# Kernel tuning notes

Hardware: AMD Instinct MI355X
Metric: run time of the kernel (lower is better)

Reference implementation:

```python
import jax, jax.numpy as jnp
import numpy as np

B, C, L = 32, 512, 16          # batch, clauses per CNF, max literals per clause
D, H, P = 256, 1024, 16        # clause_hidden_dim, hidden_size, prefix_tokens
NH, NL = 8, 4                  # adapter_heads, adapter_layers
MAXV = 512                     # max_variables


def _ln(x, w, b, eps=1e-5):
    m = jnp.mean(x, axis=-1, keepdims=True)
    v = jnp.mean(jnp.square(x - m), axis=-1, keepdims=True)
    return (x - m) * jax.lax.rsqrt(v + eps) * w + b


def _mha(q, k, v, w_in, b_in, w_out, b_out, nh):
    E = q.shape[-1]
    dh = E // nh
    wq, wk, wv = jnp.split(w_in, 3, axis=0)
    bq, bk, bv = jnp.split(b_in, 3, axis=0)

    def heads(x, w, b):
        y = x @ w.T + b
        return y.reshape(x.shape[0], x.shape[1], nh, dh).transpose(0, 2, 1, 3)

    qh, kh, vh = heads(q, wq, bq), heads(k, wk, bk), heads(v, wv, bv)
    att = jax.nn.softmax(jnp.einsum('bhqd,bhkd->bhqk', qh, kh) * (1.0 / np.sqrt(dh)), axis=-1)
    o = jnp.einsum('bhqk,bhkd->bhqd', att, vh).transpose(0, 2, 1, 3).reshape(q.shape[0], q.shape[1], E)
    return o @ w_out.T + b_out


def setup_inputs() -> dict:
    key = jax.random.key(0)
    ks = jax.random.split(key, 16)
    s = 0.02
    var_idx = jax.random.randint(ks[0], (B, C, L), 0, MAXV + 1)
    sign_idx = jax.random.randint(ks[1], (B, C, L), 1, 3)   # 1=positive literal, 2=negative
    lens = jax.random.randint(ks[2], (B, C), 1, L + 1)      # ragged clause lengths >= 1
    lit_mask = jnp.arange(L)[None, None, :] < lens[..., None]
    inp = dict(var_idx=var_idx, sign_idx=sign_idx, lit_mask=lit_mask)
    inp['var_emb'] = jax.random.normal(ks[3], (MAXV + 1, D)) * s
    inp['sign_emb'] = jax.random.normal(ks[4], (3, D)) * s
    inp['litpos_emb'] = jax.random.normal(ks[5], (L, D)) * s
    inp['clausepos_emb'] = jax.random.normal(ks[6], (C, D)) * s
    inp['enc_in_w'] = jax.random.normal(ks[7], (NL, 3 * D, D)) * s
    inp['enc_in_b'] = jnp.zeros((NL, 3 * D))
    inp['enc_out_w'] = jax.random.normal(ks[8], (NL, D, D)) * s
    inp['enc_out_b'] = jnp.zeros((NL, D))
    inp['enc_ff1_w'] = jax.random.normal(ks[9], (NL, 4 * D, D)) * s
    inp['enc_ff1_b'] = jnp.zeros((NL, 4 * D))
    inp['enc_ff2_w'] = jax.random.normal(ks[10], (NL, D, 4 * D)) * s
    inp['enc_ff2_b'] = jnp.zeros((NL, D))
    inp['enc_n1_w'] = jnp.ones((NL, D))
    inp['enc_n1_b'] = jnp.zeros((NL, D))
    inp['enc_n2_w'] = jnp.ones((NL, D))
    inp['enc_n2_b'] = jnp.zeros((NL, D))
    inp['th_ln_w'] = jnp.ones((D,))
    inp['th_ln_b'] = jnp.zeros((D,))
    inp['th_w'] = jax.random.normal(ks[11], (H, D)) * s
    inp['th_b'] = jnp.zeros((H,))
    inp['pq'] = jax.random.normal(ks[12], (P, H))
    inp['pa_in_w'] = jax.random.normal(ks[13], (3 * H, H)) * s
    inp['pa_in_b'] = jnp.zeros((3 * H,))
    inp['pa_out_w'] = jax.random.normal(ks[14], (H, H)) * s
    inp['pa_out_b'] = jnp.zeros((H,))
    inp['pn_w'] = jnp.ones((H,))
    inp['pn_b'] = jnp.zeros((H,))
    return inp


def reference(var_idx, sign_idx, lit_mask, var_emb, sign_emb, litpos_emb, clausepos_emb,
              enc_in_w, enc_in_b, enc_out_w, enc_out_b, enc_ff1_w, enc_ff1_b,
              enc_ff2_w, enc_ff2_b, enc_n1_w, enc_n1_b, enc_n2_w, enc_n2_b,
              th_ln_w, th_ln_b, th_w, th_b, pq, pa_in_w, pa_in_b, pa_out_w, pa_out_b,
              pn_w, pn_b):
    # literal states [B,C,L,D]: four embedding gathers fused into one expression
    lit = (var_emb[var_idx] + sign_emb[sign_idx]
           + litpos_emb[None, None, :, :] + clausepos_emb[None, :, None, :])
    m = lit_mask[..., None].astype(lit.dtype)
    x = jnp.sum(lit * m, axis=2) / jnp.sum(m, axis=2)   # masked mean-pool -> [B,C,D]
    for i in range(NL):  # PyTorch post-norm TransformerEncoderLayer, gelu (exact)
        a = _mha(x, x, x, enc_in_w[i], enc_in_b[i], enc_out_w[i], enc_out_b[i], NH)
        x = _ln(x + a, enc_n1_w[i], enc_n1_b[i])
        f = jax.nn.gelu(x @ enc_ff1_w[i].T + enc_ff1_b[i], approximate=False) @ enc_ff2_w[i].T + enc_ff2_b[i]
        x = _ln(x + f, enc_n2_w[i], enc_n2_b[i])
    ch = _ln(x, th_ln_w, th_ln_b) @ th_w.T + th_b       # to_hidden -> [B,C,H]
    q = jnp.broadcast_to(pq[None], (ch.shape[0], P, H))
    pref = _mha(q, ch, ch, pa_in_w, pa_in_b, pa_out_w, pa_out_b, NH)
    return _ln(pref + q, pn_w, pn_b)                    # [B,P,H]
```

## Files before the change

### kernel.cpp

```cpp
#include <hip/hip_runtime.h>
#include <hip/hip_bf16.h>

typedef unsigned short u16;
typedef unsigned int u32;
typedef __attribute__((ext_vector_type(8))) short short8;
typedef __attribute__((ext_vector_type(4))) float floatx4;

#define BB 32
#define CC 512
#define LL 16
#define DD 256
#define HH 1024
#define PP 16
#define NLAY 4

__device__ __forceinline__ float bf2f(u16 u) {
  u32 x = ((u32)u) << 16; float f; __builtin_memcpy(&f, &x, 4); return f;
}
__device__ __forceinline__ u16 f2bf(float f) {
  __hip_bfloat16 h = __float2bfloat16(f);
  u16 r; __builtin_memcpy(&r, &h, 2); return r;
}
__device__ __forceinline__ void gload_lds16(const u16* g, u16* l) {
  __builtin_amdgcn_global_load_lds(
      (const __attribute__((address_space(1))) void*)g,
      (__attribute__((address_space(3))) void*)l, 16, 0, 0);
}

__global__ __launch_bounds__(256) void cvt_kernel(
    const float* __restrict__ s0, const float* __restrict__ s1,
    const float* __restrict__ s2, const float* __restrict__ s3,
    const float* __restrict__ s4, const float* __restrict__ s5,
    const float* __restrict__ s6, const float* __restrict__ s7,
    const float* __restrict__ s8, const float* __restrict__ s9,
    const float* __restrict__ s10, const float* __restrict__ s11,
    u16* __restrict__ dst)
{
  const float* srcs[12] = {s0, s1, s2, s3, s4, s5, s6, s7, s8, s9, s10, s11};
  const int pfx[12] = {786432, 1048576, 2097152, 3145728, 3407872, 6553600, 7602176,
                       7618560, 7749888, 7750656, 7754752, 7885824};
  int e = (blockIdx.x * 256 + threadIdx.x) * 4;
  int seg = 0;
  while (e >= pfx[seg]) seg++;
  int start = seg ? pfx[seg - 1] : 0;
  float4 f = *(const float4*)(srcs[seg] + (e - start));
  u16 o[4] = {f2bf(f.x), f2bf(f.y), f2bf(f.z), f2bf(f.w)};
  *(uint2*)(dst + e) = *(const uint2*)o;
}

__global__ __launch_bounds__(256) void thwT_kernel(
    const float* __restrict__ thw, u16* __restrict__ out)
{
  __shared__ float tile[32][33];
  int bx = blockIdx.x & 7, by = blockIdx.x >> 3;
  int tx = threadIdx.x & 31, ty = threadIdx.x >> 5;
  #pragma unroll
  for (int i = 0; i < 4; ++i) {
    int h = by * 32 + ty + i * 8, d = bx * 32 + tx;
    tile[ty + i * 8][tx] = thw[h * 256 + d];
  }
  __syncthreads();
  #pragma unroll
  for (int i = 0; i < 4; ++i) {
    int d = bx * 32 + ty + i * 8, h = by * 32 + tx;
    out[d * 1024 + h] = f2bf(tile[tx][ty + i * 8]);
  }
}

__global__ __launch_bounds__(256) void bT_kernel(
    const u16* __restrict__ in, u16* __restrict__ out)
{
  __shared__ u16 tile[32][33];
  int bx = blockIdx.x & 7, by = blockIdx.x >> 3;
  int tx = threadIdx.x & 31, ty = threadIdx.x >> 5;
  #pragma unroll
  for (int i = 0; i < 4; ++i) {
    int hd = by * 32 + ty + i * 8, c = bx * 32 + tx;
    tile[ty + i * 8][tx] = in[hd * 256 + c];
  }
  __syncthreads();
  #pragma unroll
  for (int i = 0; i < 4; ++i) {
    int c = bx * 32 + ty + i * 8, hd = by * 32 + tx;
    out[c * 1024 + hd] = tile[tx][ty + i * 8];
  }
}

__global__ __launch_bounds__(256) void qc_kernel(
    const u16* __restrict__ qh, const u16* __restrict__ wckT, u16* __restrict__ qcg)
{
  int h = blockIdx.x;
  int t = threadIdx.x, lane = t & 63, w = t >> 6;
  int mrow = lane & 15, quad = lane >> 4;
  const floatx4 zf = (floatx4){0.f, 0.f, 0.f, 0.f};
  floatx4 acc[4] = {zf, zf, zf, zf};
  #pragma unroll
  for (int kk = 0; kk < 4; ++kk) {
    short8 af = *(const short8*)(qh + (size_t)mrow * 1024 + h * 128 + kk * 32 + quad * 8);
    #pragma unroll
    for (int ct = 0; ct < 4; ++ct) {
      int c = w * 64 + ct * 16 + mrow;
      short8 bf = *(const short8*)(wckT + (size_t)c * 1024 + h * 128 + kk * 32 + quad * 8);
      acc[ct] = __builtin_amdgcn_mfma_f32_16x16x32_bf16(af, bf, acc[ct], 0, 0, 0);
    }
  }
  #pragma unroll
  for (int ct = 0; ct < 4; ++ct)
    #pragma unroll
    for (int r = 0; r < 4; ++r)
      qcg[((size_t)h * 16 + quad * 4 + r) * 256 + w * 64 + ct * 16 + mrow] = f2bf(acc[ct][r]);
}

__global__ __launch_bounds__(256) void biasfold_kernel(
    const u16* __restrict__ Wkv, const float* __restrict__ thb,
    const float* __restrict__ paib, float* __restrict__ out)
{
  int wv = threadIdx.x >> 6, lane = threadIdx.x & 63;
  int n = blockIdx.x * 4 + wv;
  const u16* wr = Wkv + (size_t)n * 1024;
  float s = 0.f;
  #pragma unroll
  for (int i = 0; i < 16; ++i) {
    int h = i * 64 + lane;
    s += bf2f(wr[h]) * thb[h];
  }
  #pragma unroll
  for (int off = 32; off; off >>= 1) s += __shfl_xor(s, off);
  if (!lane) out[n] = s + paib[1024 + n];
}

__global__ __launch_bounds__(256) void redk_kernel(
    const float* __restrict__ part, const float* __restrict__ bias,
    const float* __restrict__ res, float* __restrict__ outf, u16* __restrict__ outb,
    int N, int nz, int total, int flags)
{
  int idx = (blockIdx.x * 256 + threadIdx.x) * 4;
  if (idx >= total) return;
  float4 a = *(const float4*)(part + idx);
  for (int z = 1; z < nz; ++z) {
    float4 b = *(const float4*)(part + (size_t)z * total + idx);
    a.x += b.x; a.y += b.y; a.z += b.z; a.w += b.w;
  }
  int row = idx / N, col = idx - row * N;
  float v4[4] = {a.x, a.y, a.z, a.w};
  #pragma unroll
  for (int i = 0; i < 4; ++i) {
    if (bias) v4[i] += bias[col + i];
    if (res) v4[i] += res[(size_t)((flags & 4) ? (row & 15) : row) * N + col + i];
  }
  if (outf) {
    *(float4*)(outf + idx) = *(const float4*)v4;
  } else {
    u16 o[4] = {f2bf(v4[0]), f2bf(v4[1]), f2bf(v4[2]), f2bf(v4[3])};
    *(uint2*)(outb + idx) = *(const uint2*)o;
  }
}

__global__ __launch_bounds__(256) void embed_kernel(
    const int* __restrict__ vi, const int* __restrict__ si, const int* __restrict__ mk,
    const u16* __restrict__ veb, const u16* __restrict__ seb,
    const u16* __restrict__ lpeb, const u16* __restrict__ cpeb,
    u16* __restrict__ xb)
{
  int t = threadIdx.x;
  int bc = blockIdx.x * 2 + (t >> 7);
  int c = bc & (CC - 1);
  int dl = (t & 127) * 2;
  int base = bc * LL;
  float a0 = 0.f, a1 = 0.f; int cnt = 0;
  #pragma unroll
  for (int l = 0; l < LL; ++l) {
    if (mk[base + l]) {
      int v = vi[base + l], s = si[base + l];
      u32 vv = *(const u32*)&veb[v * DD + dl];
      u32 sv = *(const u32*)&seb[s * DD + dl];
      u32 lv = *(const u32*)&lpeb[l * DD + dl];
      a0 += bf2f((u16)vv) + bf2f((u16)sv) + bf2f((u16)lv);
      a1 += bf2f((u16)(vv >> 16)) + bf2f((u16)(sv >> 16)) + bf2f((u16)(lv >> 16));
      cnt++;
    }
  }
  u32 cv = *(const u32*)&cpeb[c * DD + dl];
  float inv = 1.f / (float)cnt;
  u32 pk = (u32)f2bf(a0 * inv + bf2f((u16)cv)) | ((u32)f2bf(a1 * inv + bf2f((u16)(cv >> 16))) << 16);
  *(u32*)&xb[(size_t)bc * DD + dl] = pk;
}

template<int NC, bool GELU, bool LN, bool DLN>
__global__ __launch_bounds__(256) void gwide_kernel(
    const u16* __restrict__ A, const u16* __restrict__ W, const float* __restrict__ bias,
    const u16* __restrict__ resb, const float* __restrict__ gam, const float* __restrict__ bet,
    const float* __restrict__ gam2, const float* __restrict__ bet2,
    u16* __restrict__ out, int N, int K)
{
  constexpr int NT = NC / 32;
  constexpr int NT4 = NC / 64;
  __shared__ __align__(16) u16 As[32 * 64];
  __shared__ __align__(16) u16 Ws[NC * 64];
  __shared__ float sred[32][4][2];
  __shared__ float sred2[32][4][2];
  int t = threadIdx.x, lane = t & 63, w = t >> 6;
  int mrow = lane & 15, quad = lane >> 4;
  int bn0 = blockIdx.x * NC, bm0 = blockIdx.y * 32;

  int rA = t >> 3, gcA = (t & 7) ^ (rA & 7);
  const u16* gAp = A + (size_t)(bm0 + rA) * K + gcA * 8;
  u16* lAp = As + (w * 64) * 8;
  const u16* gW0 = W + (size_t)(bn0 + rA) * K + gcA * 8;
  u16* lW0 = Ws + (w * 64) * 8;

  floatx4 acc[2][NT4];
  #pragma unroll
  for (int mi = 0; mi < 2; ++mi)
    #pragma unroll
    for (int nt = 0; nt < NT4; ++nt) acc[mi][nt] = (floatx4){0.f, 0.f, 0.f, 0.f};

  for (int k0 = 0; k0 < K; k0 += 64) {
    __syncthreads();
    gload_lds16(gAp, lAp); gAp += 64;
    #pragma unroll
    for (int i = 0; i < NT; ++i)
      gload_lds16(gW0 + (size_t)i * 32 * K, lW0 + i * 2048);
    gW0 += 64;
    __syncthreads();
    #pragma unroll
    for (int ks = 0; ks < 2; ++ks) {
      int sw = ((ks * 4 + quad) ^ (mrow & 7)) * 8;
      short8 af0 = *(const short8*)&As[mrow * 64 + sw];
      short8 af1 = *(const short8*)&As[(16 + mrow) * 64 + sw];
      #pragma unroll
      for (int nt = 0; nt < NT4; ++nt) {
        int rw = w * (NC / 4) + nt * 16 + mrow;
        short8 bf = *(const short8*)&Ws[rw * 64 + sw];
        acc[0][nt] = __builtin_amdgcn_mfma_f32_16x16x32_bf16(af0, bf, acc[0][nt], 0, 0, 0);
        acc[1][nt] = __builtin_amdgcn_mfma_f32_16x16x32_bf16(af1, bf, acc[1][nt], 0, 0, 0);
      }
    }
  }

  if constexpr (LN) {
    float val[2][NT4][4];
    float bv[NT4];
    #pragma unroll
    for (int nt = 0; nt < NT4; ++nt) bv[nt] = bias[w * 64 + nt * 16 + mrow];
    #pragma unroll
    for (int mi = 0; mi < 2; ++mi) {
      #pragma unroll
      for (int r = 0; r < 4; ++r) {
        int gm = bm0 + mi * 16 + quad * 4 + r;
        float sr = 0.f, s2r = 0.f;
        #pragma unroll
        for (int nt = 0; nt < NT4; ++nt) {
          int gn = w * 64 + nt * 16 + mrow;
          float v = acc[mi][nt][r] + bv[nt] + bf2f(resb[(size_t)gm * 256 + gn]);
          val[mi][nt][r] = v; sr += v; s2r += v * v;
        }
        sr += __shfl_xor(sr, 1); s2r += __shfl_xor(s2r, 1);
        sr += __shfl_xor(sr, 2); s2r += __shfl_xor(s2r, 2);
        sr += __shfl_xor(sr, 4); s2r += __shfl_xor(s2r, 4);
        sr += __shfl_xor(sr, 8); s2r += __shfl_xor(s2r, 8);
        if (mrow == 0) { sred[mi * 16 + quad * 4 + r][w][0] = sr; sred[mi * 16 + quad * 4 + r][w][1] = s2r; }
      }
    }
    __syncthreads();
    #pragma unroll
    for (int mi = 0; mi < 2; ++mi) {
      #pragma unroll
      for (int r = 0; r < 4; ++r) {
        int lrow = mi * 16 + quad * 4 + r;
        float S  = sred[lrow][0][0] + sred[lrow][1][0] + sred[lrow][2][0] + sred[lrow][3][0];
        float S2 = sred[lrow][0][1] + sred[lrow][1][1] + sred[lrow][2][1] + sred[lrow][3][1];
        float mean = S * (1.f / 256.f);
        float var = S2 * (1.f / 256.f) - mean * mean;
        float inv = rsqrtf(var + 1e-5f);
        float sr2 = 0.f, s2r2 = 0.f;
        #pragma unroll
        for (int nt = 0; nt < NT4; ++nt) {
          int gn = w * 64 + nt * 16 + mrow;
          float y = (val[mi][nt][r] - mean) * inv * gam[gn] + bet[gn];
          val[mi][nt][r] = y;
          if constexpr (DLN) { sr2 += y; s2r2 += y * y; }
          else out[(size_t)(bm0 + lrow) * 256 + gn] = f2bf(y);
        }
        if constexpr (DLN) {
          sr2 += __shfl_xor(sr2, 1); s2r2 += __shfl_xor(s2r2, 1);
          sr2 += __shfl_xor(sr2, 2); s2r2 += __shfl_xor(s2r2, 2);
          sr2 += __shfl_xor(sr2, 4); s2r2 += __shfl_xor(s2r2, 4);
          sr2 += __shfl_xor(sr2, 8); s2r2 += __shfl_xor(s2r2, 8);
          if (mrow == 0) { sred2[lrow][w][0] = sr2; sred2[lrow][w][1] = s2r2; }
        }
      }
    }
    if constexpr (DLN) {
      __syncthreads();
      #pragma unroll
      for (int mi = 0; mi < 2; ++mi) {
        #pragma unroll
        for (int r = 0; r < 4; ++r) {
          int lrow = mi * 16 + quad * 4 + r;
          float S  = sred2[lrow][0][0] + sred2[lrow][1][0] + sred2[lrow][2][0] + sred2[lrow][3][0];
          float S2 = sred2[lrow][0][1] + sred2[lrow][1][1] + sred2[lrow][2][1] + sred2[lrow][3][1];
          float mean = S * (1.f / 256.f);
          float var = S2 * (1.f / 256.f) - mean * mean;
          float inv = rsqrtf(var + 1e-5f);
          #pragma unroll
          for (int nt = 0; nt < NT4; ++nt) {
            int gn = w * 64 + nt * 16 + mrow;
            float z = (val[mi][nt][r] - mean) * inv * gam2[gn] + bet2[gn];
            out[(size_t)(bm0 + lrow) * 256 + gn] = f2bf(z);
          }
        }
      }
    }
  } else {
    #pragma unroll
    for (int nt = 0; nt < NT4; ++nt) {
      int gn = bn0 + w * (NC / 4) + nt * 16 + mrow;
      float bv = bias[gn];
      #pragma unroll
      for (int mi = 0; mi < 2; ++mi) {
        #pragma unroll
        for (int r = 0; r < 4; ++r) {
          int gm = bm0 + mi * 16 + quad * 4 + r;
          float v = acc[mi][nt][r] + bv;
          if (GELU) v = 0.5f * v * (1.f + erff(v * 0.70710678118654752f));
          out[(size_t)gm * N + gn] = f2bf(v);
        }
      }
    }
  }
}

template<bool DLN>
__global__ __launch_bounds__(512) void ffu_kernel(
    const u16* __restrict__ A, const u16* __restrict__ W1, const float* __restrict__ b1,
    const u16* __restrict__ W2, const float* __restrict__ b2,
    const u16* __restrict__ resb,
    const float* __restrict__ gam, const float* __restrict__ bet,
    const float* __restrict__ gam2, const float* __restrict__ bet2,
    u16* __restrict__ out)
{
  __shared__ __align__(16) u16 As[4096];
  __shared__ __align__(16) u16 Ws[16384];
  __shared__ __align__(16) u16 Hs[4 * 4096];
  int t = threadIdx.x, lane = t & 63, w = t >> 6;
  int mrow = lane & 15, quad = lane >> 4;
  int rh = w >> 2, wc = w & 3;
  int bm0 = blockIdx.x * 64;
  int rA = t >> 3, gcA = (t & 7) ^ (rA & 7);

  floatx4 yacc[2][4];
  #pragma unroll
  for (int mi = 0; mi < 2; ++mi)
    #pragma unroll
    for (int nt = 0; nt < 4; ++nt) yacc[mi][nt] = (floatx4){0.f, 0.f, 0.f, 0.f};

  for (int nq = 0; nq < 4; ++nq) {
    floatx4 hacc[2][4];
    #pragma unroll
    for (int mi = 0; mi < 2; ++mi)
      #pragma unroll
      for (int nt = 0; nt < 4; ++nt) hacc[mi][nt] = (floatx4){0.f, 0.f, 0.f, 0.f};
    for (int kt = 0; kt < 4; ++kt) {
      __syncthreads();
      gload_lds16(A + (size_t)(bm0 + rA) * 256 + kt * 64 + gcA * 8, As + (w * 64) * 8);
      #pragma unroll
      for (int i = 0; i < 4; ++i)
        gload_lds16(W1 + (size_t)(nq * 256 + i * 64 + rA) * 256 + kt * 64 + gcA * 8,
                    Ws + i * 4096 + (w * 64) * 8);
      __syncthreads();
      #pragma unroll
      for (int ks = 0; ks < 2; ++ks) {
        int sw = ((ks * 4 + quad) ^ (mrow & 7)) * 8;
        short8 af0 = *(const short8*)&As[(rh * 32 + mrow) * 64 + sw];
        short8 af1 = *(const short8*)&As[(rh * 32 + 16 + mrow) * 64 + sw];
        #pragma unroll
        for (int nt = 0; nt < 4; ++nt) {
          short8 bf = *(const short8*)&Ws[(wc * 64 + nt * 16 + mrow) * 64 + sw];
          hacc[0][nt] = __builtin_amdgcn_mfma_f32_16x16x32_bf16(af0, bf, hacc[0][nt], 0, 0, 0);
          hacc[1][nt] = __builtin_amdgcn_mfma_f32_16x16x32_bf16(af1, bf, hacc[1][nt], 0, 0, 0);
        }
      }
    }
    {
      float bv1[4];
      #pragma unroll
      for (int nt = 0; nt < 4; ++nt) bv1[nt] = b1[nq * 256 + wc * 64 + nt * 16 + mrow];
      #pragma unroll
      for (int mi = 0; mi < 2; ++mi) {
        #pragma unroll
        for (int nt = 0; nt < 4; ++nt) {
          int g = nt * 2 + (mrow >> 3);
          #pragma unroll
          for (int r = 0; r < 4; ++r) {
            int row = rh * 32 + mi * 16 + quad * 4 + r;
            float v = hacc[mi][nt][r] + bv1[nt];
            v = 0.5f * v * (1.f + erff(v * 0.70710678118654752f));
            Hs[wc * 4096 + row * 64 + (g ^ (row & 7)) * 8 + (mrow & 7)] = f2bf(v);
          }
        }
      }
    }
    for (int kt2 = 0; kt2 < 4; ++kt2) {
      __syncthreads();
      #pragma unroll
      for (int i = 0; i < 4; ++i)
        gload_lds16(W2 + (size_t)(i * 64 + rA) * 1024 + nq * 256 + kt2 * 64 + gcA * 8,
                    Ws + i * 4096 + (w * 64) * 8);
      __syncthreads();
      #pragma unroll
      for (int ks = 0; ks < 2; ++ks) {
        int sw = ((ks * 4 + quad) ^ (mrow & 7)) * 8;
        short8 af0 = *(const short8*)&Hs[kt2 * 4096 + (rh * 32 + mrow) * 64 + sw];
        short8 af1 = *(const short8*)&Hs[kt2 * 4096 + (rh * 32 + 16 + mrow) * 64 + sw];
        #pragma unroll
        for (int nt = 0; nt < 4; ++nt) {
          short8 bf = *(const short8*)&Ws[(wc * 64 + nt * 16 + mrow) * 64 + sw];
          yacc[0][nt] = __builtin_amdgcn_mfma_f32_16x16x32_bf16(af0, bf, yacc[0][nt], 0, 0, 0);
          yacc[1][nt] = __builtin_amdgcn_mfma_f32_16x16x32_bf16(af1, bf, yacc[1][nt], 0, 0, 0);
        }
      }
    }
  }
  __syncthreads();
  float* sred  = (float*)As;
  float* sred2 = sred + 512;
  float val[2][4][4];
  float bv[4];
  #pragma unroll
  for (int nt = 0; nt < 4; ++nt) bv[nt] = b2[wc * 64 + nt * 16 + mrow];
  #pragma unroll
  for (int mi = 0; mi < 2; ++mi) {
    #pragma unroll
    for (int r = 0; r < 4; ++r) {
      int row = rh * 32 + mi * 16 + quad * 4 + r;
      int gm = bm0 + row;
      float sr = 0.f, s2r = 0.f;
      #pragma unroll
      for (int nt = 0; nt < 4; ++nt) {
        int gn = wc * 64 + nt * 16 + mrow;
        float v = yacc[mi][nt][r] + bv[nt] + bf2f(resb[(size_t)gm * 256 + gn]);
        val[mi][nt][r] = v; sr += v; s2r += v * v;
      }
      sr += __shfl_xor(sr, 1); s2r += __shfl_xor(s2r, 1);
      sr += __shfl_xor(sr, 2); s2r += __shfl_xor(s2r, 2);
      sr += __shfl_xor(sr, 4); s2r += __shfl_xor(s2r, 4);
      sr += __shfl_xor(sr, 8); s2r += __shfl_xor(s2r, 8);
      if (mrow == 0) { sred[row * 8 + wc * 2 + 0] = sr; sred[row * 8 + wc * 2 + 1] = s2r; }
    }
  }
  __syncthreads();
  #pragma unroll
  for (int mi = 0; mi < 2; ++mi) {
    #pragma unroll
    for (int r = 0; r < 4; ++r) {
      int row = rh * 32 + mi * 16 + quad * 4 + r;
      float S  = sred[row * 8 + 0] + sred[row * 8 + 2] + sred[row * 8 + 4] + sred[row * 8 + 6];
      float S2 = sred[row * 8 + 1] + sred[row * 8 + 3] + sred[row * 8 + 5] + sred[row * 8 + 7];
      float mean = S * (1.f / 256.f);
      float var = S2 * (1.f / 256.f) - mean * mean;
      float inv = rsqrtf(var + 1e-5f);
      float sr2 = 0.f, s2r2 = 0.f;
      #pragma unroll
      for (int nt = 0; nt < 4; ++nt) {
        int gn = wc * 64 + nt * 16 + mrow;
        float y = (val[mi][nt][r] - mean) * inv * gam[gn] + bet[gn];
        val[mi][nt][r] = y;
        if constexpr (DLN) { sr2 += y; s2r2 += y * y; }
        else out[(size_t)(bm0 + row) * 256 + gn] = f2bf(y);
      }
      if constexpr (DLN) {
        sr2 += __shfl_xor(sr2, 1); s2r2 += __shfl_xor(s2r2, 1);
        sr2 += __shfl_xor(sr2, 2); s2r2 += __shfl_xor(s2r2, 2);
        sr2 += __shfl_xor(sr2, 4); s2r2 += __shfl_xor(s2r2, 4);
        sr2 += __shfl_xor(sr2, 8); s2r2 += __shfl_xor(s2r2, 8);
        if (mrow == 0) { sred2[row * 8 + wc * 2 + 0] = sr2; sred2[row * 8 + wc * 2 + 1] = s2r2; }
      }
    }
  }
  if constexpr (DLN) {
    __syncthreads();
    #pragma unroll
    for (int mi = 0; mi < 2; ++mi) {
      #pragma unroll
      for (int r = 0; r < 4; ++r) {
        int row = rh * 32 + mi * 16 + quad * 4 + r;
        float S  = sred2[row * 8 + 0] + sred2[row * 8 + 2] + sred2[row * 8 + 4] + sred2[row * 8 + 6];
        float S2 = sred2[row * 8 + 1] + sred2[row * 8 + 3] + sred2[row * 8 + 5] + sred2[row * 8 + 7];
        float mean = S * (1.f / 256.f);
        float var = S2 * (1.f / 256.f) - mean * mean;
        float inv = rsqrtf(var + 1e-5f);
        #pragma unroll
        for (int nt = 0; nt < 4; ++nt) {
          int gn = wc * 64 + nt * 16 + mrow;
          float z = (val[mi][nt][r] - mean) * inv * gam2[gn] + bet2[gn];
          out[(size_t)(bm0 + row) * 256 + gn] = f2bf(z);
        }
      }
    }
  }
}

__global__ __launch_bounds__(256) void gemm128_kernel(
    const u16* __restrict__ A, const u16* __restrict__ W, const float* __restrict__ bias,
    const float* __restrict__ res, void* __restrict__ out,
    int M, int N, int K, int flags)
{
  __shared__ __align__(16) u16 As[128 * 64];
  __shared__ __align__(16) u16 Bs[128 * 64];
  int t = threadIdx.x;
  int lane = t & 63, w = t >> 6;
  int wm = w & 1, wn = w >> 1;
  int bn0 = blockIdx.x * 128, bm0 = blockIdx.y * 128;
  int mrow = lane & 15, quad = lane >> 4;
  int z = blockIdx.z, NZ = gridDim.z;
  int Kc = K / NZ, kbase = z * Kc;

  const u16* gA[4]; const u16* gB[4];
  u16* lA[4]; u16* lB[4];
  #pragma unroll
  for (int it = 0; it < 4; ++it) {
    int c = w * 256 + it * 64 + lane;
    int r = c >> 3;
    int gc = (c & 7) ^ (r & 7);
    gA[it] = A + (size_t)(bm0 + r) * K + kbase + gc * 8;
    gB[it] = W + (size_t)(bn0 + r) * K + kbase + gc * 8;
    lA[it] = As + (w * 256 + it * 64) * 8;
    lB[it] = Bs + (w * 256 + it * 64) * 8;
  }
  floatx4 acc[4][4];
  #pragma unroll
  for (int i = 0; i < 4; ++i)
    #pragma unroll
    for (int j = 0; j < 4; ++j)
      acc[i][j] = (floatx4){0.f, 0.f, 0.f, 0.f};
  int sw0 = ((0 * 4 + quad) ^ (mrow & 7)) * 8;
  int sw1 = ((1 * 4 + quad) ^ (mrow & 7)) * 8;

  for (int k0 = 0; k0 < Kc; k0 += 64) {
    __syncthreads();
    #pragma unroll
    for (int it = 0; it < 4; ++it) { gload_lds16(gA[it], lA[it]); gA[it] += 64; }
    #pragma unroll
    for (int it = 0; it < 4; ++it) { gload_lds16(gB[it], lB[it]); gB[it] += 64; }
    __syncthreads();
    #pragma unroll
    for (int ks = 0; ks < 2; ++ks) {
      int sw = ks ? sw1 : sw0;
      short8 af[4], bfr[4];
      #pragma unroll
      for (int mi = 0; mi < 4; ++mi)
        af[mi] = *(const short8*)&As[(wm * 64 + mi * 16 + mrow) * 64 + sw];
      #pragma unroll
      for (int nj = 0; nj < 4; ++nj)
        bfr[nj] = *(const short8*)&Bs[(wn * 64 + nj * 16 + mrow) * 64 + sw];
      #pragma unroll
      for (int mi = 0; mi < 4; ++mi)
        #pragma unroll
        for (int nj = 0; nj < 4; ++nj)
          acc[mi][nj] = __builtin_amdgcn_mfma_f32_16x16x32_bf16(af[mi], bfr[nj], acc[mi][nj], 0, 0, 0);
    }
  }
  if (NZ > 1) {
    float* po = (float*)out + (size_t)z * M * N;
    #pragma unroll
    for (int nj = 0; nj < 4; ++nj) {
      int gn = bn0 + wn * 64 + nj * 16 + mrow;
      #pragma unroll
      for (int mi = 0; mi < 4; ++mi)
        #pragma unroll
        for (int r = 0; r < 4; ++r) {
          int gm = bm0 + wm * 64 + mi * 16 + quad * 4 + r;
          po[(size_t)gm * N + gn] = acc[mi][nj][r];
        }
    }
    return;
  }
  bool do_gelu = (flags & 1) != 0, of32 = (flags & 2) != 0;
  #pragma unroll
  for (int nj = 0; nj < 4; ++nj) {
    int gn = bn0 + wn * 64 + nj * 16 + mrow;
    float bv = bias ? bias[gn] : 0.f;
    #pragma unroll
    for (int mi = 0; mi < 4; ++mi) {
      #pragma unroll
      for (int r = 0; r < 4; ++r) {
        int gm = bm0 + wm * 64 + mi * 16 + quad * 4 + r;
        float v = acc[mi][nj][r] + bv;
        if (do_gelu) v = 0.5f * v * (1.f + erff(v * 0.70710678118654752f));
        if (flags & 4) v += res[(size_t)(gm & 15) * N + gn];
        else if (res) v += res[(size_t)gm * N + gn];
        if (of32) ((float*)out)[(size_t)gm * N + gn] = v;
        else      ((u16*)out)[(size_t)gm * N + gn] = f2bf(v);
      }
    }
  }
}

template<int D>
__global__ __launch_bounds__(256) void lnw_kernel(
    const float* __restrict__ in, const float* __restrict__ w, const float* __restrict__ b,
    float* __restrict__ outf, u16* __restrict__ outb)
{
  constexpr int NV = D / 64;
  int lane = threadIdx.x & 63, wv = threadIdx.x >> 6;
  int row = blockIdx.x * 4 + wv;
  const float* xr = in + (size_t)row * D;
  float v[NV];
  float s = 0.f, s2 = 0.f;
  #pragma unroll
  for (int i = 0; i < NV; ++i) {
    v[i] = xr[lane + i * 64];
    s += v[i]; s2 += v[i] * v[i];
  }
  #pragma unroll
  for (int off = 32; off > 0; off >>= 1) { s += __shfl_xor(s, off); s2 += __shfl_xor(s2, off); }
  float mean = s / (float)D;
  float var = s2 / (float)D - mean * mean;
  float inv = rsqrtf(var + 1e-5f);
  #pragma unroll
  for (int i = 0; i < NV; ++i) {
    int col = lane + i * 64;
    float y = (v[i] - mean) * inv * w[col] + b[col];
    size_t o = (size_t)row * D + col;
    if (outf) outf[o] = y;
    if (outb) outb[o] = f2bf(y);
  }
}

__global__ __launch_bounds__(256, 5) void attn_enc6_kernel(
    const u16* __restrict__ qkv, u16* __restrict__ out)
{
  __shared__ __align__(16) u16 Ks[64 * 40];
  __shared__ __align__(16) u16 Vt[32 * 72];
  __shared__ __align__(16) u16 Pl[4 * 32 * 72];
  int F = blockIdx.x;
  int xcd = F & 7, jj = F >> 3;
  int pair = xcd * 32 + (jj >> 2), qt = jj & 3;
  int b = pair >> 3, h = pair & 7;
  int t = threadIdx.x, lane = t & 63, w = t >> 6;
  int mrow = lane & 15, quad = lane >> 4;
  int q0 = qt * 128 + w * 32;
  short8 qf[2];
  #pragma unroll
  for (int mi = 0; mi < 2; ++mi)
    qf[mi] = *(const short8*)(qkv + (size_t)(b * CC + q0 + mi * 16 + mrow) * 768 + h * 32 + quad * 8);
  floatx4 o[2][2];
  #pragma unroll
  for (int mi = 0; mi < 2; ++mi)
    #pragma unroll
    for (int di = 0; di < 2; ++di) o[mi][di] = (floatx4){0.f, 0.f, 0.f, 0.f};
  float lst[2][4] = {{0.f,0.f,0.f,0.f},{0.f,0.f,0.f,0.f}};
  const float sc = 0.17677669529663687f * 1.4426950408889634f;
  const floatx4 zf = (floatx4){0.f, 0.f, 0.f, 0.f};
  for (int jt = 0; jt < 8; ++jt) {
    if (jt) __syncthreads();
    {
      int j = t >> 2, q4 = (t & 3) * 8;
      uint4 kk = *(const uint4*)(qkv + (size_t)(b * CC + jt * 64 + j) * 768 + 256 + h * 32 + q4);
      *(uint4*)&Ks[j * 40 + q4] = kk;
      uint4 vv = *(const uint4*)(qkv + (size_t)(b * CC + jt * 64 + j) * 768 + 512 + h * 32 + q4);
      u16 tmp[8]; *(uint4*)tmp = vv;
      int jp = (j & 15) * 4 + (j >> 4);
      #pragma unroll
      for (int i = 0; i < 8; ++i) Vt[(q4 + i) * 72 + jp] = tmp[i];
    }
    __syncthreads();
    floatx4 s[2][4];
    #pragma unroll
    for (int nj = 0; nj < 4; ++nj) {
      short8 bf = *(const short8*)&Ks[(nj * 16 + mrow) * 40 + quad * 8];
      s[0][nj] = __builtin_amdgcn_mfma_f32_16x16x32_bf16(qf[0], bf, zf, 0, 0, 0);
      s[1][nj] = __builtin_amdgcn_mfma_f32_16x16x32_bf16(qf[1], bf, zf, 0, 0, 0);
    }
    #pragma unroll
    for (int mi = 0; mi < 2; ++mi) {
      #pragma unroll
      for (int r = 0; r < 4; ++r) {
        float ps = 0.f; u16 hv[4];
        #pragma unroll
        for (int nj = 0; nj < 4; ++nj) {
          float p = exp2f(s[mi][nj][r] * sc);
          ps += p; hv[nj] = f2bf(p);
        }
        lst[mi][r] += ps;
        *(uint2*)&Pl[(w * 32 + mi * 16 + quad * 4 + r) * 72 + mrow * 4] = *(uint2*)hv;
      }
    }
    #pragma unroll
    for (int ks = 0; ks < 2; ++ks) {
      short8 a0 = *(const short8*)&Pl[(w * 32 + mrow) * 72 + ks * 32 + quad * 8];
      short8 a1 = *(const short8*)&Pl[(w * 32 + 16 + mrow) * 72 + ks * 32 + quad * 8];
      short8 b0 = *(const short8*)&Vt[mrow * 72 + ks * 32 + quad * 8];
      short8 b1 = *(const short8*)&Vt[(16 + mrow) * 72 + ks * 32 + quad * 8];
      o[0][0] = __builtin_amdgcn_mfma_f32_16x16x32_bf16(a0, b0, o[0][0], 0, 0, 0);
      o[0][1] = __builtin_amdgcn_mfma_f32_16x16x32_bf16(a0, b1, o[0][1], 0, 0, 0);
      o[1][0] = __builtin_amdgcn_mfma_f32_16x16x32_bf16(a1, b0, o[1][0], 0, 0, 0);
      o[1][1] = __builtin_amdgcn_mfma_f32_16x16x32_bf16(a1, b1, o[1][1], 0, 0, 0);
    }
  }
  #pragma unroll
  for (int mi = 0; mi < 2; ++mi) {
    #pragma unroll
    for (int r = 0; r < 4; ++r) {
      float l = lst[mi][r];
      l += __shfl_xor(l, 1); l += __shfl_xor(l, 2);
      l += __shfl_xor(l, 4); l += __shfl_xor(l, 8);
      float inv = 1.f / l;
      int row = b * CC + q0 + mi * 16 + quad * 4 + r;
      #pragma unroll
      for (int di = 0; di < 2; ++di)
        out[(size_t)row * DD + h * 32 + di * 16 + mrow] = f2bf(o[mi][di][r] * inv);
    }
  }
}

__global__ __launch_bounds__(256) void attn_preff_kernel(
    const u16* __restrict__ tln, const u16* __restrict__ wcb,
    const u16* __restrict__ qcg, const float* __restrict__ bkv,
    u16* __restrict__ out)
{
  __shared__ __align__(16) u16 Ajc[64 * 264];
  __shared__ __align__(16) u16 Acj[256 * 72];
  __shared__ __align__(16) u16 Qs[16 * 264];
  __shared__ __align__(16) u16 Ps[16 * 72];
  __shared__ __align__(16) u16 Ts[16 * 264];
  __shared__ float Lred[4][16];
  int b = blockIdx.x, h = blockIdx.y;
  int t = threadIdx.x, lane = t & 63, w = t >> 6;
  int mrow = lane & 15, quad = lane >> 4;
  const float sc = 0.08838834764831845f * 1.4426950408889634f;
  const floatx4 zf = (floatx4){0.f, 0.f, 0.f, 0.f};
  {
    int q = t >> 4, c0 = (t & 15) * 16;
    *(uint4*)&Qs[q * 264 + c0]     = *(const uint4*)(qcg + ((size_t)h * 16 + q) * 256 + c0);
    *(uint4*)&Qs[q * 264 + c0 + 8] = *(const uint4*)(qcg + ((size_t)h * 16 + q) * 256 + c0 + 8);
  }
  floatx4 Tacc[4] = {zf, zf, zf, zf};
  float lacc = 0.f;
  const u16* tb = tln + (size_t)b * 512 * 256;
  for (int jt = 0; jt < 8; ++jt) {
    __syncthreads();
    {
      int j = t >> 2, c0 = (t & 3) * 64;
      #pragma unroll
      for (int u = 0; u < 8; ++u) {
        uint4 v = *(const uint4*)(tb + (size_t)(jt * 64 + j) * 256 + c0 + u * 8);
        *(uint4*)&Ajc[j * 264 + c0 + u * 8] = v;
        u16 tmp[8]; *(uint4*)tmp = v;
        #pragma unroll
        for (int i = 0; i < 8; ++i) Acj[(c0 + u * 8 + i) * 72 + j] = tmp[i];
      }
    }
    __syncthreads();
    floatx4 s = zf;
    #pragma unroll
    for (int kk = 0; kk < 8; ++kk) {
      short8 af = *(const short8*)&Ajc[(w * 16 + mrow) * 264 + kk * 32 + quad * 8];
      short8 bf = *(const short8*)&Qs[mrow * 264 + kk * 32 + quad * 8];
      s = __builtin_amdgcn_mfma_f32_16x16x32_bf16(af, bf, s, 0, 0, 0);
    }
    u16 hv[4]; float ps = 0.f;
    #pragma unroll
    for (int r = 0; r < 4; ++r) {
      float p = exp2f(s[r] * sc);
      ps += p; hv[r] = f2bf(p);
    }
    ps += __shfl_xor(ps, 16); ps += __shfl_xor(ps, 32);
    lacc += ps;
    *(uint2*)&Ps[mrow * 72 + w * 16 + quad * 4] = *(uint2*)hv;
    __syncthreads();
    #pragma unroll
    for (int kk = 0; kk < 2; ++kk) {
      short8 af = *(const short8*)&Ps[mrow * 72 + kk * 32 + quad * 8];
      #pragma unroll
      for (int ct = 0; ct < 4; ++ct) {
        short8 bf = *(const short8*)&Acj[(w * 64 + ct * 16 + mrow) * 72 + kk * 32 + quad * 8];
        Tacc[ct] = __builtin_amdgcn_mfma_f32_16x16x32_bf16(af, bf, Tacc[ct], 0, 0, 0);
      }
    }
  }
  if (lane < 16) Lred[w][lane] = lacc;
  __syncthreads();
  #pragma unroll
  for (int r = 0; r < 4; ++r) {
    int q = quad * 4 + r;
    float l = Lred[0][q] + Lred[1][q] + Lred[2][q] + Lred[3][q];
    float inv = 1.f / l;
    #pragma unroll
    for (int ct = 0; ct < 4; ++ct)
      Ts[q * 264 + w * 64 + ct * 16 + mrow] = f2bf(Tacc[ct][r] * inv);
  }
  __syncthreads();
  const u16* wv = wcb + (size_t)(1024 + h * 128) * 256;
  floatx4 oacc[2] = {zf, zf};
  #pragma unroll
  for (int kk = 0; kk < 8; ++kk) {
    short8 af = *(const short8*)&Ts[mrow * 264 + kk * 32 + quad * 8];
    #pragma unroll
    for (int dt = 0; dt < 2; ++dt) {
      short8 bf = *(const short8*)(wv + (size_t)(w * 32 + dt * 16 + mrow) * 256 + kk * 32 + quad * 8);
      oacc[dt] = __builtin_amdgcn_mfma_f32_16x16x32_bf16(af, bf, oacc[dt], 0, 0, 0);
    }
  }
  #pragma unroll
  for (int dt = 0; dt < 2; ++dt) {
    int d = w * 32 + dt * 16 + mrow;
    float bv = bkv[1024 + h * 128 + d];
    #pragma unroll
    for (int r = 0; r < 4; ++r) {
      int q = quad * 4 + r;
      out[((size_t)(b * 16 + q)) * 1024 + h * 128 + d] = f2bf(oacc[dt][r] + bv);
    }
  }
}

extern "C" void kernel_launch(void* const* d_in, const int* in_sizes, int n_in,
                              void* d_out, int out_size, void* d_ws, size_t ws_size,
                              hipStream_t stream)
{
  const int* vi = (const int*)d_in[0];
  const int* si = (const int*)d_in[1];
  const int* mk = (const int*)d_in[2];
  const float* ve   = (const float*)d_in[3];
  const float* se   = (const float*)d_in[4];
  const float* lpe  = (const float*)d_in[5];
  const float* cpe  = (const float*)d_in[6];
  const float* eiw  = (const float*)d_in[7];
  const float* eib  = (const float*)d_in[8];
  const float* eow  = (const float*)d_in[9];
  const float* eob  = (const float*)d_in[10];
  const float* f1w  = (const float*)d_in[11];
  const float* f1b  = (const float*)d_in[12];
  const float* f2w  = (const float*)d_in[13];
  const float* f2b  = (const float*)d_in[14];
  const float* n1w  = (const float*)d_in[15];
  const float* n1b  = (const float*)d_in[16];
  const float* n2w  = (const float*)d_in[17];
  const float* n2b  = (const float*)d_in[18];
  const float* tlw  = (const float*)d_in[19];
  const float* tlb  = (const float*)d_in[20];
  const float* thw  = (const float*)d_in[21];
  const float* thb  = (const float*)d_in[22];
  const float* pq   = (const float*)d_in[23];
  const float* paiw = (const float*)d_in[24];
  const float* paib = (const float*)d_in[25];
  const float* paow = (const float*)d_in[26];
  const float* paob = (const float*)d_in[27];
  const float* pnw  = (const float*)d_in[28];
  const float* pnb  = (const float*)d_in[29];

  const int NROW = BB * CC;
  const size_t MB = 1048576;
  char* base = (char*)d_ws;
  u16* xb   = (u16*)(base);
  u16* qkvb = (u16*)(base + 8 * MB);
  u16* atto = (u16*)(base + 32 * MB);
  u16* tln  = (u16*)(base + 96 * MB);
  u16* wcb   = (u16*)(base + 64 * MB);
  u16* thwTb = (u16*)(base + 65 * MB);
  float* bkv = (float*)(base + 66 * MB);
  u16* wckT  = (u16*)(base + 67 * MB);
  u16* qcg   = (u16*)(base + 68 * MB);
  float* skpart = (float*)(base + 80 * MB);
  u16* wbf  = (u16*)(base + 104 * MB);
  u16* qh    = (u16*)(base + 120 * MB);
  u16* prefo = (u16*)(base + 121 * MB);
  float* prefout = (float*)(base + 122 * MB);

  u16* eiw_b  = wbf + 0;
  u16* eow_b  = wbf + 786432;
  u16* f1w_b  = wbf + 1048576;
  u16* f2w_b  = wbf + 2097152;
  u16* thw_b  = wbf + 3145728;
  u16* paiw_b = wbf + 3407872;
  u16* paow_b = wbf + 6553600;
  u16* pqb    = wbf + 7602176;
  u16* veb    = wbf + 7618560;
  u16* seb    = wbf + 7749888;
  u16* lpeb   = wbf + 7750656;
  u16* cpeb   = wbf + 7754752;

  dim3 blk(256);
  dim3 blk512(512);
  cvt_kernel<<<7701, blk, 0, stream>>>(eiw, eow, f1w, f2w, thw, paiw, paow, pq,
                                       ve, se, lpe, cpe, wbf);
  thwT_kernel<<<256, blk, 0, stream>>>(thw, thwTb);
  biasfold_kernel<<<512, blk, 0, stream>>>(paiw_b + (size_t)HH * HH, thb, paib, bkv);
  gemm128_kernel<<<dim3(2, 16, 4), blk, 0, stream>>>(
      paiw_b + (size_t)HH * HH, thwTb, nullptr, nullptr, skpart, 2048, 256, HH, 0);
  redk_kernel<<<512, blk, 0, stream>>>(skpart, nullptr, nullptr, nullptr, wcb,
                                       256, 4, 2048 * 256, 0);
  gemm128_kernel<<<dim3(8, 1, 8), blk, 0, stream>>>(
      pqb, paiw_b, nullptr, nullptr, skpart, 128, 1024, HH, 0);
  redk_kernel<<<128, blk, 0, stream>>>(skpart, paib, nullptr, nullptr, qh,
                                       1024, 8, 128 * 1024, 0);
  bT_kernel<<<256, blk, 0, stream>>>(wcb, wckT);
  qc_kernel<<<8, blk, 0, stream>>>(qh, wckT, qcg);
  embed_kernel<<<NROW/2, blk, 0, stream>>>(vi, si, mk, veb, seb, lpeb, cpeb, xb);
  for (int i = 0; i < NLAY; ++i) {
    gwide_kernel<384, false, false, false><<<dim3(2, NROW/32), blk, 0, stream>>>(
        xb, eiw_b + (size_t)i*768*DD, eib + i*768, nullptr, nullptr, nullptr, nullptr, nullptr,
        qkvb, 768, DD);
    attn_enc6_kernel<<<1024, blk, 0, stream>>>(qkvb, atto);
    gwide_kernel<256, false, true, false><<<dim3(1, NROW/32), blk, 0, stream>>>(
        atto, eow_b + (size_t)i*DD*DD, eob + i*DD, xb, n1w + i*DD, n1b + i*DD, nullptr, nullptr,
        xb, DD, DD);
    if (i < NLAY - 1) {
      ffu_kernel<false><<<NROW/64, blk512, 0, stream>>>(
          xb, f1w_b + (size_t)i*HH*DD, f1b + i*HH, f2w_b + (size_t)i*DD*HH, f2b + i*DD,
          xb, n2w + i*DD, n2b + i*DD, nullptr, nullptr, xb);
    } else {
      ffu_kernel<true><<<NROW/64, blk512, 0, stream>>>(
          xb, f1w_b + (size_t)i*HH*DD, f1b + i*HH, f2w_b + (size_t)i*DD*HH, f2b + i*DD,
          xb, n2w + i*DD, n2b + i*DD, tlw, tlb, tln);
    }
  }
  attn_preff_kernel<<<dim3(BB, 8), blk, 0, stream>>>(tln, wcb, qcg, bkv, prefo);
  gemm128_kernel<<<dim3(1024/128, (BB*PP)/128, 4), blk, 0, stream>>>(
      prefo, paow_b, nullptr, nullptr, skpart, BB*PP, HH, HH, 0);
  redk_kernel<<<512, blk, 0, stream>>>(skpart, paob, pq, prefout, nullptr,
                                       1024, 4, BB*PP*HH, 4);
  lnw_kernel<1024><<<(BB*PP)/4, blk, 0, stream>>>(prefout, pnw, pnb, (float*)d_out, nullptr);
}
```

Before: 655.4 us.

## Keep FFN input tile resident in LDS and load weights two k-tiles per sync

```diff
diff --git a/kernel.cpp b/kernel.cpp
--- a/kernel.cpp
+++ b/kernel.cpp
@@ -340,8 +340,8 @@
     const float* __restrict__ gam2, const float* __restrict__ bet2,
     u16* __restrict__ out)
 {
-  __shared__ __align__(16) u16 As[4096];
-  __shared__ __align__(16) u16 Ws[16384];
+  __shared__ __align__(16) u16 Xs[4 * 4096];
+  __shared__ __align__(16) u16 Ws[2 * 16384];
   __shared__ __align__(16) u16 Hs[4 * 4096];
   int t = threadIdx.x, lane = t & 63, w = t >> 6;
   int mrow = lane & 15, quad = lane >> 4;
@@ -349,6 +349,10 @@
   int bm0 = blockIdx.x * 64;
   int rA = t >> 3, gcA = (t & 7) ^ (rA & 7);
 
+  #pragma unroll
+  for (int kt = 0; kt < 4; ++kt)
+    gload_lds16(A + (size_t)(bm0 + rA) * 256 + kt * 64 + gcA * 8, Xs + kt * 4096 + w * 512);
+
   floatx4 yacc[2][4];
   #pragma unroll
   for (int mi = 0; mi < 2; ++mi)
@@ -361,24 +365,29 @@
     for (int mi = 0; mi < 2; ++mi)
       #pragma unroll
       for (int nt = 0; nt < 4; ++nt) hacc[mi][nt] = (floatx4){0.f, 0.f, 0.f, 0.f};
-    for (int kt = 0; kt < 4; ++kt) {
+    for (int kh = 0; kh < 2; ++kh) {
       __syncthreads();
-      gload_lds16(A + (size_t)(bm0 + rA) * 256 + kt * 64 + gcA * 8, As + (w * 64) * 8);
-      #pragma unroll
-      for (int i = 0; i < 4; ++i)
-        gload_lds16(W1 + (size_t)(nq * 256 + i * 64 + rA) * 256 + kt * 64 + gcA * 8,
-                    Ws + i * 4096 + (w * 64) * 8);
+      #pragma unroll
+      for (int sub = 0; sub < 2; ++sub)
+        #pragma unroll
+        for (int i = 0; i < 4; ++i)
+          gload_lds16(W1 + (size_t)(nq * 256 + i * 64 + rA) * 256 + (kh * 2 + sub) * 64 + gcA * 8,
+                      Ws + sub * 16384 + i * 4096 + w * 512);
       __syncthreads();
       #pragma unroll
-      for (int ks = 0; ks < 2; ++ks) {
-        int sw = ((ks * 4 + quad) ^ (mrow & 7)) * 8;
-        short8 af0 = *(const short8*)&As[(rh * 32 + mrow) * 64 + sw];
-        short8 af1 = *(const short8*)&As[(rh * 32 + 16 + mrow) * 64 + sw];
-        #pragma unroll
-        for (int nt = 0; nt < 4; ++nt) {
-          short8 bf = *(const short8*)&Ws[(wc * 64 + nt * 16 + mrow) * 64 + sw];
-          hacc[0][nt] = __builtin_amdgcn_mfma_f32_16x16x32_bf16(af0, bf, hacc[0][nt], 0, 0, 0);
-          hacc[1][nt] = __builtin_amdgcn_mfma_f32_16x16x32_bf16(af1, bf, hacc[1][nt], 0, 0, 0);
+      for (int sub = 0; sub < 2; ++sub) {
+        int kt = kh * 2 + sub;
+        #pragma unroll
+        for (int ks = 0; ks < 2; ++ks) {
+          int sw = ((ks * 4 + quad) ^ (mrow & 7)) * 8;
+          short8 af0 = *(const short8*)&Xs[kt * 4096 + (rh * 32 + mrow) * 64 + sw];
+          short8 af1 = *(const short8*)&Xs[kt * 4096 + (rh * 32 + 16 + mrow) * 64 + sw];
+          #pragma unroll
+          for (int nt = 0; nt < 4; ++nt) {
+            short8 bf = *(const short8*)&Ws[sub * 16384 + (wc * 64 + nt * 16 + mrow) * 64 + sw];
+            hacc[0][nt] = __builtin_amdgcn_mfma_f32_16x16x32_bf16(af0, bf, hacc[0][nt], 0, 0, 0);
+            hacc[1][nt] = __builtin_amdgcn_mfma_f32_16x16x32_bf16(af1, bf, hacc[1][nt], 0, 0, 0);
+          }
         }
       }
     }
@@ -401,29 +410,35 @@
         }
       }
     }
-    for (int kt2 = 0; kt2 < 4; ++kt2) {
+    for (int kh = 0; kh < 2; ++kh) {
       __syncthreads();
       #pragma unroll
-      for (int i = 0; i < 4; ++i)
-        gload_lds16(W2 + (size_t)(i * 64 + rA) * 1024 + nq * 256 + kt2 * 64 + gcA * 8,
-                    Ws + i * 4096 + (w * 64) * 8);
+      for (int sub = 0; sub < 2; ++sub)
+        #pragma unroll
+        for (int i = 0; i < 4; ++i)
+          gload_lds16(W2 + (size_t)(i * 64 + rA) * 1024 + nq * 256 + (kh * 2 + sub) * 64 + gcA * 8,
+                      Ws + sub * 16384 + i * 4096 + w * 512);
       __syncthreads();
       #pragma unroll
-      for (int ks = 0; ks < 2; ++ks) {
-        int sw = ((ks * 4 + quad) ^ (mrow & 7)) * 8;
-        short8 af0 = *(const short8*)&Hs[kt2 * 4096 + (rh * 32 + mrow) * 64 + sw];
-        short8 af1 = *(const short8*)&Hs[kt2 * 4096 + (rh * 32 + 16 + mrow) * 64 + sw];
-        #pragma unroll
-        for (int nt = 0; nt < 4; ++nt) {
-          short8 bf = *(const short8*)&Ws[(wc * 64 + nt * 16 + mrow) * 64 + sw];
-          yacc[0][nt] = __builtin_amdgcn_mfma_f32_16x16x32_bf16(af0, bf, yacc[0][nt], 0, 0, 0);
-          yacc[1][nt] = __builtin_amdgcn_mfma_f32_16x16x32_bf16(af1, bf, yacc[1][nt], 0, 0, 0);
+      for (int sub = 0; sub < 2; ++sub) {
+        int kt2 = kh * 2 + sub;
+        #pragma unroll
+        for (int ks = 0; ks < 2; ++ks) {
+          int sw = ((ks * 4 + quad) ^ (mrow & 7)) * 8;
+          short8 af0 = *(const short8*)&Hs[kt2 * 4096 + (rh * 32 + mrow) * 64 + sw];
+          short8 af1 = *(const short8*)&Hs[kt2 * 4096 + (rh * 32 + 16 + mrow) * 64 + sw];
+          #pragma unroll
+          for (int nt = 0; nt < 4; ++nt) {
+            short8 bf = *(const short8*)&Ws[sub * 16384 + (wc * 64 + nt * 16 + mrow) * 64 + sw];
+            yacc[0][nt] = __builtin_amdgcn_mfma_f32_16x16x32_bf16(af0, bf, yacc[0][nt], 0, 0, 0);
+            yacc[1][nt] = __builtin_amdgcn_mfma_f32_16x16x32_bf16(af1, bf, yacc[1][nt], 0, 0, 0);
+          }
         }
       }
     }
   }
   __syncthreads();
-  float* sred  = (float*)As;
+  float* sred  = (float*)Xs;
   float* sred2 = sred + 512;
   float val[2][4][4];
   float bv[4];
```

Measured after the change: 643.9 us. Within noise of the previous version (-1.8%).
